# Kernel tuning notes

Hardware: AMD Instinct MI355X
Metric: run time of the kernel (lower is better)

Reference implementation:

```python
import jax, jax.numpy as jnp
import numpy as np

HIGHEST = jax.lax.Precision.HIGHEST
KEY_CHUNK_SIZE = 4096 * 4  # hard-coded in the module's __call__
HEADS = 8
DIM_HEAD = 64


def _query_chunk_size(num_q: int) -> int:
    # replicates the module's static chunk-size selection
    if num_q % 64 == 0:
        return num_q // 64
    if num_q % 16 == 0:
        return num_q // 16
    if num_q % 4 == 0:
        return num_q // 4
    return num_q


def _me_attention(q, k, v, q_chunk: int, k_chunk: int):
    # q, k, v: (S, H, D) where H here is the flattened batch*heads axis
    S, H, D = q.shape
    num_kv = k.shape[0]
    k_chunk = min(k_chunk, num_kv)
    q = q / jnp.sqrt(jnp.asarray(D, q.dtype))
    kc = k.reshape(-1, k_chunk, H, D)          # (nk, kc, H, D)
    vc = v.reshape(-1, k_chunk, H, v.shape[-1])

    def per_qchunk(qch):  # qch: (qc, H, D)
        def summarize(args):
            kch, vch = args
            s = jnp.einsum('qhd,khd->qhk', qch, kch, precision=HIGHEST)
            m = jax.lax.stop_gradient(jnp.max(s, axis=-1, keepdims=True))
            e = jnp.exp(s - m)
            ev = jnp.einsum('khf,qhk->qhf', vch, e, precision=HIGHEST)
            return ev, e.sum(axis=-1), m[..., 0]
        evs, ews, ms = jax.lax.map(summarize, (kc, vc))  # stacked over key chunks
        gm = jnp.max(ms, axis=0)                # (qc, H) global running max
        sc = jnp.exp(ms - gm)                   # (nk, qc, H) rescale factors
        num = (evs * sc[..., None]).sum(axis=0)
        den = (ews * sc).sum(axis=0)
        return num / den[..., None]

    qs = q.reshape(-1, q_chunk, H, D)
    out = jax.lax.map(per_qchunk, qs)           # (nq, qc, H, F)
    return out.reshape(S, H, -1)


def _forward(hidden_states, w_q, w_k, w_v, w_out, b_out):
    B, S, Dm = hidden_states.shape
    H, dh = HEADS, DIM_HEAD
    q = hidden_states @ w_q
    k = hidden_states @ w_k
    v = hidden_states @ w_v

    def to_heads(t):  # (B,S,H*dh) -> (B*H, S, dh)
        return t.reshape(B, S, H, dh).transpose(0, 2, 1, 3).reshape(B * H, S, dh)

    qs, ks, vs = to_heads(q), to_heads(k), to_heads(v)
    # module transposes to (S, B*H, dh) before memory-efficient attention
    qcs = _query_chunk_size(S)
    attn = _me_attention(qs.transpose(1, 0, 2), ks.transpose(1, 0, 2),
                         vs.transpose(1, 0, 2), qcs, KEY_CHUNK_SIZE)
    attn = attn.transpose(1, 0, 2)  # (B*H, S, dh)
    attn = attn.reshape(B, H, S, dh).transpose(0, 2, 1, 3).reshape(B, S, H * dh)
    return attn @ w_out + b_out


def setup_inputs() -> dict:
    key = jax.random.key(0)
    ks = jax.random.split(key, 6)
    B, S, Dm = 2, 8192, 512
    inner = HEADS * DIM_HEAD  # 512
    return {
        'hidden_states': jax.random.normal(ks[0], (B, S, Dm), dtype=jnp.float32),
        'w_q': jax.random.normal(ks[1], (Dm, inner), dtype=jnp.float32) * 0.02,
        'w_k': jax.random.normal(ks[2], (Dm, inner), dtype=jnp.float32) * 0.02,
        'w_v': jax.random.normal(ks[3], (Dm, inner), dtype=jnp.float32) * 0.02,
        'w_out': jax.random.normal(ks[4], (inner, Dm), dtype=jnp.float32) * 0.02,
        'b_out': jnp.zeros((Dm,), dtype=jnp.float32),
    }


def reference(hidden_states, w_q, w_k, w_v, w_out, b_out):
    return _forward(hidden_states, w_q, w_k, w_v, w_out, b_out)
```

## Files before the change

### kernel.cpp

```cpp
#include <hip/hip_runtime.h>
#include <stdint.h>

typedef unsigned short u16;
typedef __attribute__((ext_vector_type(8))) short short8;
typedef __attribute__((ext_vector_type(4))) float f32x4;
typedef __attribute__((ext_vector_type(16))) float f32x16;

#define MFMA32(a, b, c) __builtin_amdgcn_mfma_f32_16x16x32_bf16(a, b, c, 0, 0, 0)
#define MFMA3232(a, b, c) __builtin_amdgcn_mfma_f32_32x32x16_bf16(a, b, c, 0, 0, 0)

#if __has_builtin(__builtin_amdgcn_exp2f)
#define EXP2F(x) __builtin_amdgcn_exp2f(x)
#else
#define EXP2F(x) exp2f(x)
#endif

#define ASYNC16(G, L)                                                            \
    __builtin_amdgcn_global_load_lds((const __attribute__((address_space(1))) void*)(const void*)(G), \
                                     (__attribute__((address_space(3))) void*)(void*)(L), 16, 0, 0)

__device__ __forceinline__ u16 f2bf(float f) {
    union { float f; uint32_t u; } c; c.f = f;
    uint32_t r = (c.u + 0x7fffu + ((c.u >> 16) & 1u)) >> 16;
    return (u16)r;
}

__global__ __launch_bounds__(256) void k_convert_w(const float* __restrict__ W0, const float* __restrict__ W1,
                                                   const float* __restrict__ W2, const float* __restrict__ W3,
                                                   u16* __restrict__ Wt) {
    __shared__ u16 T[64][72];
    const float* W = (blockIdx.z == 0) ? W0 : (blockIdx.z == 1) ? W1 : (blockIdx.z == 2) ? W2 : W3;
    int k0 = blockIdx.x * 64, n0 = blockIdx.y * 64;
    int t = threadIdx.x;
    for (int i = 0; i < 4; i++) {
        int id = t + i * 256;
        int row = id >> 4, c4 = (id & 15) * 4;
        float4 v = *(const float4*)(W + (size_t)(k0 + row) * 512 + n0 + c4);
        union { u16 s[4]; uint2 v; } u;
        u.s[0] = f2bf(v.x); u.s[1] = f2bf(v.y); u.s[2] = f2bf(v.z); u.s[3] = f2bf(v.w);
        *(uint2*)&T[row][c4] = u.v;
    }
    __syncthreads();
    u16* O = Wt + (size_t)blockIdx.z * 512 * 512;
    for (int i = 0; i < 2; i++) {
        int id = t + i * 256;
        int row = id >> 3, c8 = (id & 7) * 8;
        union { u16 s[8]; uint4 v; } tmp;
        for (int j = 0; j < 8; j++) tmp.s[j] = T[c8 + j][row];
        *(uint4*)(O + (size_t)(n0 + row) * 512 + k0 + c8) = tmp.v;
    }
}

__global__ __launch_bounds__(256) void k_gemm_qkv(const float* __restrict__ X, const u16* __restrict__ Wt,
                                                  u16* __restrict__ Q, u16* __restrict__ K, u16* __restrict__ V) {
    __shared__ u16 As[128][40];
    __shared__ u16 Bs[128][40];
    const int t = threadIdx.x;
    const int wave = t >> 6, lane = t & 63, quad = lane >> 4, l16 = lane & 15;
    const int wm = (wave >> 1) * 64, wn = (wave & 1) * 64;
    const int m0 = blockIdx.x * 128, n0 = blockIdx.y * 128;
    const u16* Bt = Wt + (size_t)blockIdx.z * 262144;
    const f32x4 fz = {0.f, 0.f, 0.f, 0.f};
    f32x4 acc[4][4];
    for (int i = 0; i < 4; i++) for (int j = 0; j < 4; j++) acc[i][j] = fz;
    for (int k0 = 0; k0 < 512; k0 += 32) {
        __syncthreads();
        for (int i = 0; i < 2; i++) {
            int id = t + i * 256;
            int row = id >> 2, c8 = (id & 3) * 8;
            float4 xa = *(const float4*)(X + (size_t)(m0 + row) * 512 + k0 + c8);
            float4 xb = *(const float4*)(X + (size_t)(m0 + row) * 512 + k0 + c8 + 4);
            union { u16 s[8]; uint4 v; } ux;
            ux.s[0] = f2bf(xa.x); ux.s[1] = f2bf(xa.y); ux.s[2] = f2bf(xa.z); ux.s[3] = f2bf(xa.w);
            ux.s[4] = f2bf(xb.x); ux.s[5] = f2bf(xb.y); ux.s[6] = f2bf(xb.z); ux.s[7] = f2bf(xb.w);
            *(uint4*)&As[row][c8] = ux.v;
            *(uint4*)&Bs[row][c8] = *(const uint4*)(Bt + (size_t)(n0 + row) * 512 + k0 + c8);
        }
        __syncthreads();
        short8 af[4], bf[4];
        for (int mt = 0; mt < 4; mt++) af[mt] = *(const short8*)&As[wm + mt * 16 + l16][quad * 8];
        for (int nt = 0; nt < 4; nt++) bf[nt] = *(const short8*)&Bs[wn + nt * 16 + l16][quad * 8];
        for (int mt = 0; mt < 4; mt++)
            for (int nt = 0; nt < 4; nt++)
                acc[mt][nt] = MFMA32(af[mt], bf[nt], acc[mt][nt]);
    }
    const float scale = (blockIdx.z == 0) ? 0.18033688011112042f : 1.0f;
    u16* Out = (blockIdx.z == 0) ? Q : (blockIdx.z == 1) ? K : V;
    for (int mt = 0; mt < 4; mt++)
        for (int nt = 0; nt < 4; nt++)
            for (int r = 0; r < 4; r++) {
                int m = m0 + wm + mt * 16 + quad * 4 + r;
                int n = n0 + wn + nt * 16 + l16;
                int b = m >> 13, s = m & 8191, h = n >> 6, d = n & 63;
                Out[((size_t)((b * 8 + h) * 8192 + s)) * 64 + d] = f2bf(acc[mt][nt][r] * scale);
            }
}

__global__ __launch_bounds__(256) void k_transpose_v(const u16* __restrict__ V, u16* __restrict__ Vt) {
    __shared__ u16 T[64][72];
    int s0 = blockIdx.x * 64, bh = blockIdx.y;
    int t = threadIdx.x;
    for (int i = 0; i < 2; i++) {
        int id = t + i * 256, row = id >> 3, c8 = (id & 7) * 8;
        *(uint4*)&T[row][c8] = *(const uint4*)(V + ((size_t)bh * 8192 + s0 + row) * 64 + c8);
    }
    __syncthreads();
    for (int i = 0; i < 2; i++) {
        int id = t + i * 256, row = id >> 3, c8 = (id & 7) * 8;
        union { u16 s[8]; uint4 v; } tmp;
        for (int j = 0; j < 8; j++) tmp.s[j] = T[c8 + j][row];
        *(uint4*)(Vt + ((size_t)bh * 64 + row) * 8192 + s0 + c8) = tmp.v;
    }
}

__global__ __launch_bounds__(512, 4) void k_flash(const u16* __restrict__ Q, const u16* __restrict__ K,
                                                  const u16* __restrict__ Vt, u16* __restrict__ Attn) {
    __shared__ u16 KsAll[2][4096];
    __shared__ u16 VsAll[2][4096];
    const int t = threadIdx.x;
    const int wave = t >> 6, lane = t & 63;
    const int l32 = lane & 31, hi = lane >> 5;
    const int s7 = l32 & 7;
    const int qblk = blockIdx.x, bh = blockIdx.y;
    const int b = bh >> 3, h = bh & 7;
    const int q0g = qblk * 256;
    const int mq = wave * 32;
    const u16* Qb = Q + ((size_t)bh * 8192 + q0g) * 64;
    const u16* Kb = K + (size_t)bh * 8192 * 64;
    const u16* Vb = Vt + (size_t)bh * 64 * 8192;

    const int r0 = t >> 3;
    const int pr = (r0 & 3) | ((r0 & 4) << 1) | ((r0 & 8) >> 1) | (r0 & 48);
    const int x0K = ((t & 7) ^ (r0 & 7)) * 8;
    const int x0V = ((t & 7) ^ (r0 & 7)) * 8;
    const u16* gK0 = Kb + pr * 64 + x0K;
    const u16* gV0 = Vb + (size_t)r0 * 8192 + x0V;
    u16* lK = &KsAll[0][0] + t * 8;
    u16* lV = &VsAll[0][0] + t * 8;

    auto prefetch = [&](int it, int buf) {
        ASYNC16(gK0 + it * 4096, lK + buf * 4096);
        ASYNC16(gV0 + it * 64,   lV + buf * 4096);
    };

    short8 qf[4];
    for (int g = 0; g < 4; g++)
        qf[g] = *(const short8*)(Qb + (size_t)(mq + l32) * 64 + g * 16 + hi * 8);

    const f32x16 fz16 = {};
    f32x16 o0 = {}, o1 = {};
    float l_i = 0.f;

    prefetch(0, 0);

    auto body = [&](int it, int buf) {
        __syncthreads();
        if (it != 127) prefetch(it + 1, buf ^ 1);
        const u16* KsB = &KsAll[buf][0];
        const u16* VsB = &VsAll[buf][0];

        const u16* K0 = KsB + l32 * 64;
        const u16* K1 = K0 + 2048;
        f32x16 s0, s1;
        s0 = MFMA3232(*(const short8*)(K0 + ((0 + hi) ^ s7) * 8), qf[0], fz16);
        s0 = MFMA3232(*(const short8*)(K0 + ((2 + hi) ^ s7) * 8), qf[1], s0);
        s0 = MFMA3232(*(const short8*)(K0 + ((4 + hi) ^ s7) * 8), qf[2], s0);
        s0 = MFMA3232(*(const short8*)(K0 + ((6 + hi) ^ s7) * 8), qf[3], s0);
        s1 = MFMA3232(*(const short8*)(K1 + ((0 + hi) ^ s7) * 8), qf[0], fz16);
        s1 = MFMA3232(*(const short8*)(K1 + ((2 + hi) ^ s7) * 8), qf[1], s1);
        s1 = MFMA3232(*(const short8*)(K1 + ((4 + hi) ^ s7) * 8), qf[2], s1);
        s1 = MFMA3232(*(const short8*)(K1 + ((6 + hi) ^ s7) * 8), qf[3], s1);

        union fu { float f; uint32_t u; };
        uint32_t w[2][8];
#pragma unroll
        for (int j = 0; j < 8; j++) {
            fu a, c; a.f = EXP2F(s0[2 * j]); c.f = EXP2F(s0[2 * j + 1]);
            l_i += a.f + c.f;
            w[0][j] = __builtin_amdgcn_perm(c.u, a.u, 0x07060302);
        }
#pragma unroll
        for (int j = 0; j < 8; j++) {
            fu a, c; a.f = EXP2F(s1[2 * j]); c.f = EXP2F(s1[2 * j + 1]);
            l_i += a.f + c.f;
            w[1][j] = __builtin_amdgcn_perm(c.u, a.u, 0x07060302);
        }

        const u16* V0 = VsB + l32 * 64;
        const u16* V1 = V0 + 2048;
#pragma unroll
        for (int f = 0; f < 4; f++) {
            union { uint32_t u[4]; short8 s; } pk;
            pk.u[0] = w[f >> 1][4 * (f & 1) + 0];
            pk.u[1] = w[f >> 1][4 * (f & 1) + 1];
            pk.u[2] = w[f >> 1][4 * (f & 1) + 2];
            pk.u[3] = w[f >> 1][4 * (f & 1) + 3];
            short8 va = *(const short8*)(V0 + ((2 * f + hi) ^ s7) * 8);
            short8 vb = *(const short8*)(V1 + ((2 * f + hi) ^ s7) * 8);
            o0 = MFMA3232(pk.s, va, o0);
            o1 = MFMA3232(pk.s, vb, o1);
        }
    };

    for (int it2 = 0; it2 < 64; it2++) {
        body(2 * it2, 0);
        body(2 * it2 + 1, 1);
    }

    l_i += __shfl_xor(l_i, 32);
    float inv = 1.0f / l_i;
#pragma unroll
    for (int reg = 0; reg < 16; reg++) {
        int qrow = (reg & 3) + 8 * (reg >> 2) + 4 * hi;
        float iv = __shfl(inv, qrow);
        int sg = q0g + mq + qrow;
        size_t base = ((size_t)(b * 8192 + sg)) * 512 + h * 64;
        Attn[base + l32]      = f2bf(o0[reg] * iv);
        Attn[base + 32 + l32] = f2bf(o1[reg] * iv);
    }
}

__global__ __launch_bounds__(256) void k_gemm_out(const u16* __restrict__ A, const u16* __restrict__ Wot,
                                                  const float* __restrict__ bias, float* __restrict__ Out) {
    __shared__ u16 As[128][40];
    __shared__ u16 Bs[128][40];
    const int t = threadIdx.x;
    const int wave = t >> 6, lane = t & 63, quad = lane >> 4, l16 = lane & 15;
    const int wm = (wave >> 1) * 64, wn = (wave & 1) * 64;
    const int m0 = blockIdx.x * 128, n0 = blockIdx.y * 128;
    const f32x4 fz = {0.f, 0.f, 0.f, 0.f};
    f32x4 acc[4][4];
    for (int i = 0; i < 4; i++) for (int j = 0; j < 4; j++) acc[i][j] = fz;
    for (int k0 = 0; k0 < 512; k0 += 32) {
        __syncthreads();
        for (int i = 0; i < 2; i++) {
            int id = t + i * 256;
            int row = id >> 2, c8 = (id & 3) * 8;
            *(uint4*)&As[row][c8] = *(const uint4*)(A + (size_t)(m0 + row) * 512 + k0 + c8);
            *(uint4*)&Bs[row][c8] = *(const uint4*)(Wot + (size_t)(n0 + row) * 512 + k0 + c8);
        }
        __syncthreads();
        short8 af[4], bf[4];
        for (int mt = 0; mt < 4; mt++) af[mt] = *(const short8*)&As[wm + mt * 16 + l16][quad * 8];
        for (int nt = 0; nt < 4; nt++) bf[nt] = *(const short8*)&Bs[wn + nt * 16 + l16][quad * 8];
        for (int mt = 0; mt < 4; mt++)
            for (int nt = 0; nt < 4; nt++)
                acc[mt][nt] = MFMA32(af[mt], bf[nt], acc[mt][nt]);
    }
    float bv[4];
    for (int nt = 0; nt < 4; nt++) bv[nt] = bias[n0 + wn + nt * 16 + l16];
    for (int mt = 0; mt < 4; mt++)
        for (int nt = 0; nt < 4; nt++)
            for (int r = 0; r < 4; r++) {
                int m = m0 + wm + mt * 16 + quad * 4 + r;
                int n = n0 + wn + nt * 16 + l16;
                Out[(size_t)m * 512 + n] = acc[mt][nt][r] + bv[nt];
            }
}

extern "C" void kernel_launch(void* const* d_in, const int* in_sizes, int n_in,
                              void* d_out, int out_size, void* d_ws, size_t ws_size,
                              hipStream_t stream) {
    const float* X   = (const float*)d_in[0];
    const float* w_q = (const float*)d_in[1];
    const float* w_k = (const float*)d_in[2];
    const float* w_v = (const float*)d_in[3];
    const float* w_o = (const float*)d_in[4];
    const float* b_o = (const float*)d_in[5];
    float* Out = (float*)d_out;

    char* ws = (char*)d_ws;
    u16* Attn = (u16*)(ws);
    u16* Wt   = (u16*)(ws + 16777216);
    u16* Qd   = (u16*)(ws + 18874368);
    u16* Kd   = (u16*)(ws + 35651584);
    u16* Vd   = (u16*)(ws + 52428800);
    u16* Vtd  = (u16*)(ws + 69206016);

    hipLaunchKernelGGL(k_convert_w, dim3(8, 8, 4), dim3(256), 0, stream, w_q, w_k, w_v, w_o, Wt);
    hipLaunchKernelGGL(k_gemm_qkv, dim3(128, 4, 3), dim3(256), 0, stream, X, Wt, Qd, Kd, Vd);
    hipLaunchKernelGGL(k_transpose_v, dim3(128, 16), dim3(256), 0, stream, Vd, Vtd);
    hipLaunchKernelGGL(k_flash, dim3(32, 16), dim3(512), 0, stream, Qd, Kd, Vtd, Attn);
    hipLaunchKernelGGL(k_gemm_out, dim3(128, 4), dim3(256), 0, stream, Attn, Wt + 3 * 262144, b_o, Out);
}
```

Baseline: 407.6 us.

## Fuse V transpose into QKV GEMM, pre-convert X to bf16, add MFMA priority

Adds a kernel that converts X to bf16 once, so the QKV GEMM no longer re-reads and re-converts fp32 X for each of its N tiles. The V-transpose kernel is removed: V blocks now stage their tile through shared memory and write the transposed layout directly. The flash kernel raises wave priority around its MFMA sections with s_setprio. This saves one kernel launch and one V round trip, but adds a conversion kernel and extra barriers in the V epilogue.

```diff
diff --git a/kernel.cpp b/kernel.cpp
--- a/kernel.cpp
+++ b/kernel.cpp
@@ -23,6 +23,14 @@
     union { float f; uint32_t u; } c; c.f = f;
     uint32_t r = (c.u + 0x7fffu + ((c.u >> 16) & 1u)) >> 16;
     return (u16)r;
+}
+
+__global__ __launch_bounds__(256) void k_convert_x(const float* __restrict__ X, u16* __restrict__ Xb) {
+    int idx = blockIdx.x * 256 + threadIdx.x;
+    float4 v = ((const float4*)X)[idx];
+    union { u16 s[4]; uint2 v; } u;
+    u.s[0] = f2bf(v.x); u.s[1] = f2bf(v.y); u.s[2] = f2bf(v.z); u.s[3] = f2bf(v.w);
+    ((uint2*)Xb)[idx] = u.v;
 }
 
 __global__ __launch_bounds__(256) void k_convert_w(const float* __restrict__ W0, const float* __restrict__ W1,
@@ -51,10 +59,12 @@
     }
 }
 
-__global__ __launch_bounds__(256) void k_gemm_qkv(const float* __restrict__ X, const u16* __restrict__ Wt,
-                                                  u16* __restrict__ Q, u16* __restrict__ K, u16* __restrict__ V) {
-    __shared__ u16 As[128][40];
-    __shared__ u16 Bs[128][40];
+__global__ __launch_bounds__(256) void k_gemm_qkv(const u16* __restrict__ X, const u16* __restrict__ Wt,
+                                                  u16* __restrict__ Q, u16* __restrict__ K, u16* __restrict__ Vt) {
+    __shared__ u16 pool[10240];
+    u16 (*As)[40] = (u16(*)[40])pool;
+    u16 (*Bs)[40] = (u16(*)[40])(pool + 5120);
+    u16 (*Tv)[72] = (u16(*)[72])pool;
     const int t = threadIdx.x;
     const int wave = t >> 6, lane = t & 63, quad = lane >> 4, l16 = lane & 15;
     const int wm = (wave >> 1) * 64, wn = (wave & 1) * 64;
@@ -68,12 +78,7 @@
         for (int i = 0; i < 2; i++) {
             int id = t + i * 256;
             int row = id >> 2, c8 = (id & 3) * 8;
-            float4 xa = *(const float4*)(X + (size_t)(m0 + row) * 512 + k0 + c8);
-            float4 xb = *(const float4*)(X + (size_t)(m0 + row) * 512 + k0 + c8 + 4);
-            union { u16 s[8]; uint4 v; } ux;
-            ux.s[0] = f2bf(xa.x); ux.s[1] = f2bf(xa.y); ux.s[2] = f2bf(xa.z); ux.s[3] = f2bf(xa.w);
-            ux.s[4] = f2bf(xb.x); ux.s[5] = f2bf(xb.y); ux.s[6] = f2bf(xb.z); ux.s[7] = f2bf(xb.w);
-            *(uint4*)&As[row][c8] = ux.v;
+            *(uint4*)&As[row][c8] = *(const uint4*)(X + (size_t)(m0 + row) * 512 + k0 + c8);
             *(uint4*)&Bs[row][c8] = *(const uint4*)(Bt + (size_t)(n0 + row) * 512 + k0 + c8);
         }
         __syncthreads();
@@ -84,8 +89,30 @@
             for (int nt = 0; nt < 4; nt++)
                 acc[mt][nt] = MFMA32(af[mt], bf[nt], acc[mt][nt]);
     }
+    if (blockIdx.z == 2) {
+        const int b = m0 >> 13, s0 = m0 & 8191;
+        const int h0 = n0 >> 6;
+        for (int p = 0; p < 2; p++) {
+            __syncthreads();
+            if ((wave & 1) == p) {
+                for (int mt = 0; mt < 4; mt++)
+                    for (int nt = 0; nt < 4; nt++)
+                        for (int r = 0; r < 4; r++)
+                            Tv[wm + mt * 16 + quad * 4 + r][nt * 16 + l16] = f2bf(acc[mt][nt][r]);
+            }
+            __syncthreads();
+            int d = t >> 2, so = (t & 3) * 32;
+            u16* dst = Vt + ((size_t)((b * 8 + h0 + p) * 64 + d)) * 8192 + s0 + so;
+            for (int j = 0; j < 4; j++) {
+                union { u16 s[8]; uint4 v; } tmp;
+                for (int k = 0; k < 8; k++) tmp.s[k] = Tv[so + j * 8 + k][d];
+                *(uint4*)(dst + j * 8) = tmp.v;
+            }
+        }
+        return;
+    }
     const float scale = (blockIdx.z == 0) ? 0.18033688011112042f : 1.0f;
-    u16* Out = (blockIdx.z == 0) ? Q : (blockIdx.z == 1) ? K : V;
+    u16* Out = (blockIdx.z == 0) ? Q : K;
     for (int mt = 0; mt < 4; mt++)
         for (int nt = 0; nt < 4; nt++)
             for (int r = 0; r < 4; r++) {
@@ -94,23 +121,6 @@
                 int b = m >> 13, s = m & 8191, h = n >> 6, d = n & 63;
                 Out[((size_t)((b * 8 + h) * 8192 + s)) * 64 + d] = f2bf(acc[mt][nt][r] * scale);
             }
-}
-
-__global__ __launch_bounds__(256) void k_transpose_v(const u16* __restrict__ V, u16* __restrict__ Vt) {
-    __shared__ u16 T[64][72];
-    int s0 = blockIdx.x * 64, bh = blockIdx.y;
-    int t = threadIdx.x;
-    for (int i = 0; i < 2; i++) {
-        int id = t + i * 256, row = id >> 3, c8 = (id & 7) * 8;
-        *(uint4*)&T[row][c8] = *(const uint4*)(V + ((size_t)bh * 8192 + s0 + row) * 64 + c8);
-    }
-    __syncthreads();
-    for (int i = 0; i < 2; i++) {
-        int id = t + i * 256, row = id >> 3, c8 = (id & 7) * 8;
-        union { u16 s[8]; uint4 v; } tmp;
-        for (int j = 0; j < 8; j++) tmp.s[j] = T[c8 + j][row];
-        *(uint4*)(Vt + ((size_t)bh * 64 + row) * 8192 + s0 + c8) = tmp.v;
-    }
 }
 
 __global__ __launch_bounds__(512, 4) void k_flash(const u16* __restrict__ Q, const u16* __restrict__ K,
@@ -162,6 +172,7 @@
         const u16* K0 = KsB + l32 * 64;
         const u16* K1 = K0 + 2048;
         f32x16 s0, s1;
+        __builtin_amdgcn_s_setprio(1);
         s0 = MFMA3232(*(const short8*)(K0 + ((0 + hi) ^ s7) * 8), qf[0], fz16);
         s0 = MFMA3232(*(const short8*)(K0 + ((2 + hi) ^ s7) * 8), qf[1], s0);
         s0 = MFMA3232(*(const short8*)(K0 + ((4 + hi) ^ s7) * 8), qf[2], s0);
@@ -170,6 +181,7 @@
         s1 = MFMA3232(*(const short8*)(K1 + ((2 + hi) ^ s7) * 8), qf[1], s1);
         s1 = MFMA3232(*(const short8*)(K1 + ((4 + hi) ^ s7) * 8), qf[2], s1);
         s1 = MFMA3232(*(const short8*)(K1 + ((6 + hi) ^ s7) * 8), qf[3], s1);
+        __builtin_amdgcn_s_setprio(0);
 
         union fu { float f; uint32_t u; };
         uint32_t w[2][8];
@@ -188,6 +200,7 @@
 
         const u16* V0 = VsB + l32 * 64;
         const u16* V1 = V0 + 2048;
+        __builtin_amdgcn_s_setprio(1);
 #pragma unroll
         for (int f = 0; f < 4; f++) {
             union { uint32_t u[4]; short8 s; } pk;
@@ -200,6 +213,7 @@
             o0 = MFMA3232(pk.s, va, o0);
             o1 = MFMA3232(pk.s, vb, o1);
         }
+        __builtin_amdgcn_s_setprio(0);
     };
 
     for (int it2 = 0; it2 < 64; it2++) {
@@ -270,16 +284,16 @@
     float* Out = (float*)d_out;
 
     char* ws = (char*)d_ws;
-    u16* Attn = (u16*)(ws);
+    u16* Xb   = (u16*)(ws);
     u16* Wt   = (u16*)(ws + 16777216);
     u16* Qd   = (u16*)(ws + 18874368);
     u16* Kd   = (u16*)(ws + 35651584);
-    u16* Vd   = (u16*)(ws + 52428800);
-    u16* Vtd  = (u16*)(ws + 69206016);
-
+    u16* Vtd  = (u16*)(ws + 52428800);
+    u16* Attn = Xb;
+
+    hipLaunchKernelGGL(k_convert_x, dim3(8192), dim3(256), 0, stream, X, Xb);
     hipLaunchKernelGGL(k_convert_w, dim3(8, 8, 4), dim3(256), 0, stream, w_q, w_k, w_v, w_o, Wt);
-    hipLaunchKernelGGL(k_gemm_qkv, dim3(128, 4, 3), dim3(256), 0, stream, X, Wt, Qd, Kd, Vd);
-    hipLaunchKernelGGL(k_transpose_v, dim3(128, 16), dim3(256), 0, stream, Vd, Vtd);
+    hipLaunchKernelGGL(k_gemm_qkv, dim3(128, 4, 3), dim3(256), 0, stream, Xb, Wt, Qd, Kd, Vtd);
     hipLaunchKernelGGL(k_flash, dim3(32, 16), dim3(512), 0, stream, Qd, Kd, Vtd, Attn);
     hipLaunchKernelGGL(k_gemm_out, dim3(128, 4), dim3(256), 0, stream, Attn, Wt + 3 * 262144, b_o, Out);
 }
```

After: 426.2 us. 1.05x slower.
